# Kernel optimization log

Hardware: AMD Instinct MI355X
Metric: run time of the kernel (lower is better)

Reference implementation:

```python
import jax, jax.numpy as jnp
import numpy as np

NUM_CLASSES = 1000
FEAT_DIM = 256
N = 262144
ALPHA = 0.5


def setup_inputs() -> dict:
    key = jax.random.key(0)
    k1, k2, k3 = jax.random.split(key, 3)
    features = jax.random.normal(k1, (N, FEAT_DIM), dtype=jnp.float32)
    labels = jax.random.randint(k2, (N,), 0, NUM_CLASSES, dtype=jnp.int64)
    centers = jax.random.normal(k3, (NUM_CLASSES, FEAT_DIM), dtype=jnp.float32)
    return {"features": features, "labels": labels, "centers": centers}


def reference(features, labels, centers):
    # Fused segment-mean: scatter-add of features + per-class counts,
    # replacing the per-class python loop in the original.
    sums = jax.ops.segment_sum(features, labels, num_segments=NUM_CLASSES)  # [C, D]
    counts = jax.ops.segment_sum(
        jnp.ones((features.shape[0],), dtype=features.dtype),
        labels,
        num_segments=NUM_CLASSES,
    )  # [C]
    has_samples = counts > 0
    safe_counts = jnp.where(has_samples, counts, 1.0)
    class_means = sums / safe_counts[:, None]  # [C, D]
    # EMA update only for classes present in the batch.
    updated = (1.0 - ALPHA) * centers + ALPHA * class_means
    new_centers = jnp.where(has_samples[:, None], updated, centers)
    return new_centers
```

## Files before the change

### kernel.cpp

```cpp
#include <hip/hip_runtime.h>

constexpr int N    = 262144;
constexpr int C    = 1000;
constexpr int D    = 256;
constexpr int D4   = 64;
constexpr int CPAD = 1024;
constexpr int NB   = 64;
constexpr int ROWS_PER_B = N / NB;
constexpr float ALPHA = 0.5f;

typedef float vfloat4 __attribute__((ext_vector_type(4)));


__global__ __launch_bounds__(256) void hist_kernel(
        const int* __restrict__ labels, int* __restrict__ hist,
        float4* __restrict__ sums4) {
    __shared__ int h[CPAD];
    int t = threadIdx.x;
    for (int i = t; i < CPAD; i += 256) h[i] = 0;
    for (int i = blockIdx.x * 256 + t; i < C * D / 4; i += NB * 256)
        sums4[i] = float4{0.f, 0.f, 0.f, 0.f};
    __syncthreads();
    int base = blockIdx.x * ROWS_PER_B;
    for (int i = t; i < ROWS_PER_B; i += 256)
        atomicAdd(&h[labels[base + i]], 1);
    __syncthreads();
    int* out = hist + blockIdx.x * CPAD;
    for (int i = t; i < CPAD; i += 256) out[i] = h[i];
}

__global__ __launch_bounds__(1024) void scan_kernel(
        const int* __restrict__ hist,
        int* __restrict__ counts,
        int* __restrict__ blockcursor) {
    __shared__ int s[CPAD];
    int t = threadIdx.x;
    int total = 0;
    #pragma unroll 8
    for (int b = 0; b < NB; ++b) total += hist[b * CPAD + t];
    counts[t] = total;
    s[t] = total;
    __syncthreads();
    for (int off = 1; off < CPAD; off <<= 1) {
        int add = (t >= off) ? s[t - off] : 0;
        __syncthreads();
        s[t] += add;
        __syncthreads();
    }
    int run = s[t] - total;
    #pragma unroll 4
    for (int b = 0; b < NB; ++b) {
        blockcursor[b * CPAD + t] = run;
        run += hist[b * CPAD + t];
    }
}

__global__ __launch_bounds__(256) void scatter_kernel(
        const int* __restrict__ labels,
        const int* __restrict__ blockcursor,
        int* __restrict__ S) {
    __shared__ int cur[CPAD];
    int t = threadIdx.x;
    const int* bc = blockcursor + blockIdx.x * CPAD;
    for (int i = t; i < CPAD; i += 256) cur[i] = bc[i];
    __syncthreads();
    int base = blockIdx.x * ROWS_PER_B;
    for (int i = t; i < ROWS_PER_B; i += 256) {
        int row = base + i;
        int lab = labels[row];
        int pos = atomicAdd(&cur[lab], 1);
        S[pos] = (row << 10) | lab;
    }
}

__global__ __launch_bounds__(256) void seg_reduce_kernel(
        const vfloat4* __restrict__ feat4,
        const int* __restrict__ S,
        float* __restrict__ sums) {
    int wave = threadIdx.x >> 6;
    int lane = threadIdx.x & 63;
    int base = (blockIdx.x * 4 + wave) * 64;
    int packed = S[base + lane];

    vfloat4 acc = (vfloat4)0.f;
    int cur = __shfl(packed, 0) & 1023;

    constexpr int PF = 8;
    int pk[PF];
    vfloat4 v[PF];
    #pragma unroll
    for (int j = 0; j < PF; ++j) {
        pk[j] = __shfl(packed, j);
        v[j]  = __builtin_nontemporal_load(&feat4[(long)(pk[j] >> 10) * D4 + lane]);
    }
    #pragma unroll
    for (int i = 0; i < 64; i += PF) {
        int npk[PF];
        vfloat4 nv[PF];
        if (i + PF < 64) {
            #pragma unroll
            for (int j = 0; j < PF; ++j) {
                npk[j] = __shfl(packed, i + PF + j);
                nv[j]  = __builtin_nontemporal_load(&feat4[(long)(npk[j] >> 10) * D4 + lane]);
            }
        }
        #pragma unroll
        for (int j = 0; j < PF; ++j) {
            int lab = pk[j] & 1023;
            if (lab != cur) {
                float* dst = sums + cur * D + lane * 4;
                unsafeAtomicAdd(dst + 0, acc.x);
                unsafeAtomicAdd(dst + 1, acc.y);
                unsafeAtomicAdd(dst + 2, acc.z);
                unsafeAtomicAdd(dst + 3, acc.w);
                acc = (vfloat4)0.f;
                cur = lab;
            }
            acc += v[j];
        }
        #pragma unroll
        for (int j = 0; j < PF; ++j) { pk[j] = npk[j]; v[j] = nv[j]; }
    }
    float* dst = sums + cur * D + lane * 4;
    unsafeAtomicAdd(dst + 0, acc.x);
    unsafeAtomicAdd(dst + 1, acc.y);
    unsafeAtomicAdd(dst + 2, acc.z);
    unsafeAtomicAdd(dst + 3, acc.w);
}

__global__ __launch_bounds__(256) void ema_kernel(
        const float4* __restrict__ cen4,
        const float* __restrict__ sums,
        const int* __restrict__ counts,
        float4* __restrict__ out4) {
    int idx = blockIdx.x * 256 + threadIdx.x;
    if (idx >= C * D4) return;
    int c = idx >> 6;
    int cnt = counts[c];
    float4 cen = cen4[idx];
    float4 o = cen;
    if (cnt > 0) {
        const float* sp = sums + c * D + (idx & 63) * 4;
        float s = ALPHA / (float)cnt;
        o.x = (1.0f - ALPHA) * cen.x + sp[0] * s;
        o.y = (1.0f - ALPHA) * cen.y + sp[1] * s;
        o.z = (1.0f - ALPHA) * cen.z + sp[2] * s;
        o.w = (1.0f - ALPHA) * cen.w + sp[3] * s;
    }
    out4[idx] = o;
}

extern "C" void kernel_launch(void* const* d_in, const int* in_sizes, int n_in,
                              void* d_out, int out_size, void* d_ws, size_t ws_size,
                              hipStream_t stream) {
    const vfloat4* feat4  = (const vfloat4*)d_in[0];
    const int*     labels = (const int*)d_in[1];
    const float4*  cen4   = (const float4*)d_in[2];
    float4*        out4   = (float4*)d_out;

    int*   hist        = (int*)d_ws;
    int*   counts      = hist + NB * CPAD;
    int*   blockcursor = counts + CPAD;
    int*   S           = blockcursor + NB * CPAD;
    float* sums        = (float*)(S + N);

    hist_kernel<<<NB, 256, 0, stream>>>(labels, hist, (float4*)sums);
    scan_kernel<<<1, CPAD, 0, stream>>>(hist, counts, blockcursor);
    scatter_kernel<<<NB, 256, 0, stream>>>(labels, blockcursor, S);
    seg_reduce_kernel<<<N / 256, 256, 0, stream>>>(feat4, S, sums);
    ema_kernel<<<(C * D4 + 255) / 256, 256, 0, stream>>>(cen4, sums, counts, out4);
}
```

Baseline: 367.2 us.

## Fuse scan into scatter kernel and simplify seg-reduce load batching

Removes the single-block scan kernel: each scatter block now reads the full histogram, computes per-class totals and its own block prefix, and runs the exclusive scan redundantly in shared memory. This drops one launch and the blockcursor round trip through global memory, at the cost of every block repeating the scan work and reading all of hist. Seg-reduce also replaces its software-pipelined double-buffered prefetch with a simpler non-unrolled loop that issues 8 loads and then consumes them, which cuts register pressure but may expose more memory latency.

Result: no change. 368.0 us (+0.2%).

```diff
diff --git a/kernel.cpp b/kernel.cpp
--- a/kernel.cpp
+++ b/kernel.cpp
@@ -29,46 +29,54 @@
     for (int i = t; i < CPAD; i += 256) out[i] = h[i];
 }
 
-__global__ __launch_bounds__(1024) void scan_kernel(
+__global__ __launch_bounds__(256) void scatter_kernel(
+        const int* __restrict__ labels,
         const int* __restrict__ hist,
         int* __restrict__ counts,
-        int* __restrict__ blockcursor) {
+        int* __restrict__ S) {
     __shared__ int s[CPAD];
+    __shared__ int cu[CPAD];
     int t = threadIdx.x;
-    int total = 0;
-    #pragma unroll 8
-    for (int b = 0; b < NB; ++b) total += hist[b * CPAD + t];
-    counts[t] = total;
-    s[t] = total;
+    int myb = blockIdx.x;
+
+    int tot[4] = {0, 0, 0, 0};
+    int pre[4] = {0, 0, 0, 0};
+    for (int b = 0; b < NB; ++b) {
+        #pragma unroll
+        for (int c = 0; c < 4; ++c) {
+            int v = hist[b * CPAD + c * 256 + t];
+            tot[c] += v;
+            if (b < myb) pre[c] += v;
+        }
+    }
+    #pragma unroll
+    for (int c = 0; c < 4; ++c) s[c * 256 + t] = tot[c];
     __syncthreads();
     for (int off = 1; off < CPAD; off <<= 1) {
-        int add = (t >= off) ? s[t - off] : 0;
+        int add[4];
+        #pragma unroll
+        for (int c = 0; c < 4; ++c) {
+            int idx = c * 256 + t;
+            add[c] = (idx >= off) ? s[idx - off] : 0;
+        }
         __syncthreads();
-        s[t] += add;
+        #pragma unroll
+        for (int c = 0; c < 4; ++c) s[c * 256 + t] += add[c];
         __syncthreads();
     }
-    int run = s[t] - total;
-    #pragma unroll 4
-    for (int b = 0; b < NB; ++b) {
-        blockcursor[b * CPAD + t] = run;
-        run += hist[b * CPAD + t];
+    #pragma unroll
+    for (int c = 0; c < 4; ++c) {
+        int idx = c * 256 + t;
+        cu[idx] = s[idx] - tot[c] + pre[c];
+        if (myb == 0) counts[idx] = tot[c];
     }
-}
+    __syncthreads();
 
-__global__ __launch_bounds__(256) void scatter_kernel(
-        const int* __restrict__ labels,
-        const int* __restrict__ blockcursor,
-        int* __restrict__ S) {
-    __shared__ int cur[CPAD];
-    int t = threadIdx.x;
-    const int* bc = blockcursor + blockIdx.x * CPAD;
-    for (int i = t; i < CPAD; i += 256) cur[i] = bc[i];
-    __syncthreads();
-    int base = blockIdx.x * ROWS_PER_B;
+    int base = myb * ROWS_PER_B;
     for (int i = t; i < ROWS_PER_B; i += 256) {
         int row = base + i;
         int lab = labels[row];
-        int pos = atomicAdd(&cur[lab], 1);
+        int pos = atomicAdd(&cu[lab], 1);
         S[pos] = (row << 10) | lab;
     }
 }
@@ -85,27 +93,17 @@
     vfloat4 acc = (vfloat4)0.f;
     int cur = __shfl(packed, 0) & 1023;
 
-    constexpr int PF = 8;
-    int pk[PF];
-    vfloat4 v[PF];
-    #pragma unroll
-    for (int j = 0; j < PF; ++j) {
-        pk[j] = __shfl(packed, j);
-        v[j]  = __builtin_nontemporal_load(&feat4[(long)(pk[j] >> 10) * D4 + lane]);
-    }
-    #pragma unroll
-    for (int i = 0; i < 64; i += PF) {
-        int npk[PF];
-        vfloat4 nv[PF];
-        if (i + PF < 64) {
-            #pragma unroll
-            for (int j = 0; j < PF; ++j) {
-                npk[j] = __shfl(packed, i + PF + j);
-                nv[j]  = __builtin_nontemporal_load(&feat4[(long)(npk[j] >> 10) * D4 + lane]);
-            }
-        }
+    #pragma unroll 1
+    for (int i = 0; i < 64; i += 8) {
+        int pk[8];
+        vfloat4 v[8];
         #pragma unroll
-        for (int j = 0; j < PF; ++j) {
+        for (int j = 0; j < 8; ++j) pk[j] = __shfl(packed, i + j);
+        #pragma unroll
+        for (int j = 0; j < 8; ++j)
+            v[j] = __builtin_nontemporal_load(&feat4[(long)(pk[j] >> 10) * D4 + lane]);
+        #pragma unroll
+        for (int j = 0; j < 8; ++j) {
             int lab = pk[j] & 1023;
             if (lab != cur) {
                 float* dst = sums + cur * D + lane * 4;
@@ -118,8 +116,6 @@
             }
             acc += v[j];
         }
-        #pragma unroll
-        for (int j = 0; j < PF; ++j) { pk[j] = npk[j]; v[j] = nv[j]; }
     }
     float* dst = sums + cur * D + lane * 4;
     unsafeAtomicAdd(dst + 0, acc.x);
@@ -158,15 +154,13 @@
     const float4*  cen4   = (const float4*)d_in[2];
     float4*        out4   = (float4*)d_out;
 
-    int*   hist        = (int*)d_ws;
-    int*   counts      = hist + NB * CPAD;
-    int*   blockcursor = counts + CPAD;
-    int*   S           = blockcursor + NB * CPAD;
-    float* sums        = (float*)(S + N);
+    int*   hist   = (int*)d_ws;
+    int*   counts = hist + NB * CPAD;
+    int*   S      = counts + CPAD;
+    float* sums   = (float*)(S + N);
 
     hist_kernel<<<NB, 256, 0, stream>>>(labels, hist, (float4*)sums);
-    scan_kernel<<<1, CPAD, 0, stream>>>(hist, counts, blockcursor);
-    scatter_kernel<<<NB, 256, 0, stream>>>(labels, blockcursor, S);
+    scatter_kernel<<<NB, 256, 0, stream>>>(labels, hist, counts, S);
     seg_reduce_kernel<<<N / 256, 256, 0, stream>>>(feat4, S, sums);
     ema_kernel<<<(C * D4 + 255) / 256, 256, 0, stream>>>(cen4, sums, counts, out4);
 }
```
